# Performance work log

Measured on AMD Instinct MI355X. Metric: run time of the kernel, lower is better.

The kernel has to match this reference:

```python
import math
import jax, jax.numpy as jnp
import numpy as np

B, S, D = 2, 2048, 4096
H, KVH = 32, 8
HD = D // H            # 128
REP = H // KVH         # 4


def setup_inputs() -> dict:
    key = jax.random.key(0)
    ks = jax.random.split(key, 7)
    scale = 1.0 / math.sqrt(D)
    return {
        "x": jax.random.normal(ks[0], (B, S, D), dtype=jnp.float32),
        "freqs_cos": jax.random.uniform(ks[1], (S, HD // 2), dtype=jnp.float32),
        "freqs_sin": jax.random.uniform(ks[2], (S, HD // 2), dtype=jnp.float32),
        "Wq": jax.random.normal(ks[3], (D, H * HD), dtype=jnp.float32) * scale,
        "Wk": jax.random.normal(ks[4], (D, KVH * HD), dtype=jnp.float32) * scale,
        "Wv": jax.random.normal(ks[5], (D, KVH * HD), dtype=jnp.float32) * scale,
        "Wo": jax.random.normal(ks[6], (H * HD, D), dtype=jnp.float32) * scale,
    }


def _rope(t, cos, sin):
    # t: [B,S,h,HD]; pairs are interleaved (reshape to (HD//2, 2) in original)
    tr = t[..., 0::2]
    ti = t[..., 1::2]
    cos = cos[None, :, None, :]  # [1,S,1,HD//2]
    sin = sin[None, :, None, :]
    out_r = tr * cos - ti * sin
    out_i = tr * sin + ti * cos
    return jnp.stack([out_r, out_i], axis=-1).reshape(t.shape)


def reference(x, freqs_cos, freqs_sin, Wq, Wk, Wv, Wo):
    b, s, _ = x.shape
    xq = (x @ Wq).reshape(b, s, H, HD)
    xk = (x @ Wk).reshape(b, s, KVH, HD)
    xv = (x @ Wv).reshape(b, s, KVH, HD)

    xq = _rope(xq, freqs_cos, freqs_sin)
    xk = _rope(xk, freqs_cos, freqs_sin)

    # GQA: repeat each kv head REP times -> [b,s,H,HD]
    xk = jnp.repeat(xk, REP, axis=2)
    xv = jnp.repeat(xv, REP, axis=2)

    q = xq.transpose(0, 2, 1, 3)  # [b,H,s,HD]
    k = xk.transpose(0, 2, 1, 3)
    v = xv.transpose(0, 2, 1, 3)

    scores = jnp.einsum('bhqd,bhkd->bhqk', q, k) / math.sqrt(HD)
    causal = jnp.tril(jnp.ones((s, s), dtype=bool))
    scores = jnp.where(causal[None, None], scores, jnp.float32(-jnp.inf))
    probs = jax.nn.softmax(scores.astype(jnp.float32), axis=-1).astype(x.dtype)

    out = jnp.einsum('bhqk,bhkd->bhqd', probs, v)
    out = out.transpose(0, 2, 1, 3).reshape(b, s, H * HD)
    return out @ Wo
```

## Files before the change

### kernel.cpp

```cpp
#include <hip/hip_runtime.h>

typedef unsigned short u16;
typedef unsigned int u32;
typedef __attribute__((ext_vector_type(8))) short bf16x8;
typedef __attribute__((ext_vector_type(8))) unsigned short u16x8;
typedef __attribute__((ext_vector_type(4))) unsigned short u16x4;
typedef __attribute__((ext_vector_type(4))) float f32x4;
typedef __attribute__((ext_vector_type(4))) unsigned int u32x4;

#define S_LEN 2048
#define NB 2
#define NH 32
#define NKVH 8
#define HD 128
#define DMODEL 4096
#define NEG_BIG (-1.0e30f)

__device__ __forceinline__ float bf2f(u16 x) {
  union { u32 u; float f; } v; v.u = ((u32)x) << 16; return v.f;
}
__device__ __forceinline__ u16 f2bf(float f) {
  union { float f; u32 u; } v; v.f = f;
  u32 r = v.u + 0x7FFFu + ((v.u >> 16) & 1u);
  return (u16)(r >> 16);
}

__global__ __launch_bounds__(256) void transpose_w(const float* __restrict__ W,
                                                   u16* __restrict__ out,
                                                   int N)
{
  __shared__ u16 Ls[64 * 68];
  const int t  = threadIdx.x;
  const int k0 = blockIdx.x * 64;
  const int n0 = blockIdx.y * 64;
#pragma unroll
  for (int i = 0; i < 4; ++i) {
    int kr = (t >> 4) + i * 16;
    int nc = (t & 15) * 4;
    f32x4 v = *(const f32x4*)&W[(size_t)(k0 + kr) * N + n0 + nc];
    u16x4 h = { f2bf(v[0]), f2bf(v[1]), f2bf(v[2]), f2bf(v[3]) };
    *(u16x4*)&Ls[kr * 68 + nc] = h;
  }
  __syncthreads();
#pragma unroll
  for (int i = 0; i < 2; ++i) {
    int nr = (t >> 3) + i * 32;
    int kc = (t & 7) * 8;
    u16x8 h;
#pragma unroll
    for (int j = 0; j < 8; ++j) h[j] = Ls[(kc + j) * 68 + nr];
    *(u16x8*)&out[(size_t)(n0 + nr) * 4096 + k0 + kc] = h;
  }
}

__global__ __launch_bounds__(256) void gemm_qkv(const float* __restrict__ A,
                                                const u16* __restrict__ Bt,
                                                u16* __restrict__ Yq,
                                                u16* __restrict__ Yk,
                                                u16* __restrict__ Yv)
{
  __shared__ u16 As[128 * 40];
  __shared__ u16 Bs[128 * 40];
  const int tid  = threadIdx.x;
  const int wave = tid >> 6;
  const int lane = tid & 63;
  const int lr   = lane & 15;
  const int quad = lane >> 4;
  const int wm   = (wave >> 1) * 64;
  const int wn   = (wave & 1) * 64;
  const int bm   = blockIdx.y * 128;
  const int bn   = blockIdx.x * 128;

  const f32x4 zero = {0.f, 0.f, 0.f, 0.f};
  f32x4 acc[4][4];
#pragma unroll
  for (int i = 0; i < 4; ++i)
#pragma unroll
    for (int j = 0; j < 4; ++j) acc[i][j] = zero;

  for (int kt = 0; kt < 4096; kt += 32) {
    __syncthreads();
#pragma unroll
    for (int i = 0; i < 4; ++i) {
      int e = (tid + i * 256) * 4;
      int row = e >> 5, col = e & 31;
      f32x4 v = *(const f32x4*)&A[(size_t)(bm + row) * 4096 + kt + col];
      u16x4 h = { f2bf(v[0]), f2bf(v[1]), f2bf(v[2]), f2bf(v[3]) };
      *(u16x4*)&As[row * 40 + col] = h;
    }
#pragma unroll
    for (int i = 0; i < 2; ++i) {
      int e = (tid + i * 256) * 8;
      int nr = e >> 5, kc = e & 31;
      *(u32x4*)&Bs[nr * 40 + kc] =
          *(const u32x4*)&Bt[(size_t)(bn + nr) * 4096 + kt + kc];
    }
    __syncthreads();

    bf16x8 af[4], bfr[4];
#pragma unroll
    for (int mt = 0; mt < 4; ++mt)
      af[mt] = *(const bf16x8*)&As[(wm + mt * 16 + lr) * 40 + quad * 8];
#pragma unroll
    for (int nt = 0; nt < 4; ++nt)
      bfr[nt] = *(const bf16x8*)&Bs[(wn + nt * 16 + lr) * 40 + quad * 8];
#pragma unroll
    for (int mt = 0; mt < 4; ++mt)
#pragma unroll
      for (int nt = 0; nt < 4; ++nt)
        acc[mt][nt] = __builtin_amdgcn_mfma_f32_16x16x32_bf16(af[mt], bfr[nt], acc[mt][nt], 0, 0, 0);
  }

  u16* dst; size_t ldc; int nbase;
  if (bn < 4096)      { dst = Yq; ldc = 4096; nbase = bn; }
  else if (bn < 5120) { dst = Yk; ldc = 1024; nbase = bn - 4096; }
  else                { dst = Yv; ldc = 1024; nbase = bn - 5120; }
#pragma unroll
  for (int mt = 0; mt < 4; ++mt)
#pragma unroll
    for (int nt = 0; nt < 4; ++nt)
#pragma unroll
      for (int r = 0; r < 4; ++r) {
        size_t m = (size_t)(bm + wm + mt * 16 + quad * 4 + r);
        size_t n = (size_t)(nbase + wn + nt * 16 + lr);
        dst[m * ldc + n] = f2bf(acc[mt][nt][r]);
      }
}

__global__ __launch_bounds__(256) void gemm_o(const u16* __restrict__ A,
                                              const u16* __restrict__ Bt,
                                              float* __restrict__ C)
{
  __shared__ u16 As[128 * 40];
  __shared__ u16 Bs[128 * 40];
  const int tid  = threadIdx.x;
  const int wave = tid >> 6;
  const int lane = tid & 63;
  const int lr   = lane & 15;
  const int quad = lane >> 4;
  const int wm   = (wave >> 1) * 64;
  const int wn   = (wave & 1) * 64;
  const int bm   = blockIdx.y * 128;
  const int bn   = blockIdx.x * 128;

  const f32x4 zero = {0.f, 0.f, 0.f, 0.f};
  f32x4 acc[4][4];
#pragma unroll
  for (int i = 0; i < 4; ++i)
#pragma unroll
    for (int j = 0; j < 4; ++j) acc[i][j] = zero;

  for (int kt = 0; kt < 4096; kt += 32) {
    __syncthreads();
#pragma unroll
    for (int i = 0; i < 2; ++i) {
      int e = (tid + i * 256) * 8;
      int row = e >> 5, col = e & 31;
      *(u32x4*)&As[row * 40 + col] =
          *(const u32x4*)&A[(size_t)(bm + row) * 4096 + kt + col];
    }
#pragma unroll
    for (int i = 0; i < 2; ++i) {
      int e = (tid + i * 256) * 8;
      int nr = e >> 5, kc = e & 31;
      *(u32x4*)&Bs[nr * 40 + kc] =
          *(const u32x4*)&Bt[(size_t)(bn + nr) * 4096 + kt + kc];
    }
    __syncthreads();

    bf16x8 af[4], bfr[4];
#pragma unroll
    for (int mt = 0; mt < 4; ++mt)
      af[mt] = *(const bf16x8*)&As[(wm + mt * 16 + lr) * 40 + quad * 8];
#pragma unroll
    for (int nt = 0; nt < 4; ++nt)
      bfr[nt] = *(const bf16x8*)&Bs[(wn + nt * 16 + lr) * 40 + quad * 8];
#pragma unroll
    for (int mt = 0; mt < 4; ++mt)
#pragma unroll
      for (int nt = 0; nt < 4; ++nt)
        acc[mt][nt] = __builtin_amdgcn_mfma_f32_16x16x32_bf16(af[mt], bfr[nt], acc[mt][nt], 0, 0, 0);
  }

#pragma unroll
  for (int mt = 0; mt < 4; ++mt)
#pragma unroll
    for (int nt = 0; nt < 4; ++nt)
#pragma unroll
      for (int r = 0; r < 4; ++r) {
        size_t m = (size_t)(bm + wm + mt * 16 + quad * 4 + r);
        size_t n = (size_t)(bn + wn + nt * 16 + lr);
        C[m * 4096 + n] = acc[mt][nt][r];
      }
}

__global__ __launch_bounds__(256) void rope_kernel(u16* __restrict__ Y,
                                                   const float* __restrict__ cp,
                                                   const float* __restrict__ sp,
                                                   int log2nh, int total)
{
  int idx = blockIdx.x * 256 + threadIdx.x;
  if (idx >= total) return;
  int j = idx & 63;
  int s = (idx >> (6 + log2nh)) & (S_LEN - 1);
  u16 t0 = Y[(size_t)idx * 2];
  u16 t1 = Y[(size_t)idx * 2 + 1];
  float tr = bf2f(t0), ti = bf2f(t1);
  float c  = cp[s * 64 + j];
  float sn = sp[s * 64 + j];
  Y[(size_t)idx * 2]     = f2bf(tr * c - ti * sn);
  Y[(size_t)idx * 2 + 1] = f2bf(tr * sn + ti * c);
}

__global__ __launch_bounds__(256) void attn_kernel(const u16* Q,
                                                   const u16* __restrict__ K,
                                                   const u16* __restrict__ V,
                                                   u16* O)
{
  __shared__ u16 Ks[64 * 136];
  __shared__ u16 Vs[128 * 72];
  __shared__ u16 Ps[4 * 16 * 72];

  const int tid  = threadIdx.x;
  const int wave = tid >> 6;
  const int lane = tid & 63;
  const int lr   = lane & 15;
  const int quad = lane >> 4;

  const int b   = blockIdx.z;
  const int h   = blockIdx.y;
  const int q0  = ((int)gridDim.x - 1 - (int)blockIdx.x) * 64;
  const int kvh = h >> 2;

  const int qrow = q0 + wave * 16 + lr;
  const u16* qptr = Q + ((size_t)((b * S_LEN + qrow) * NH + h)) * HD;
  bf16x8 aq[4];
#pragma unroll
  for (int c = 0; c < 4; ++c) aq[c] = *(const bf16x8*)(qptr + c * 32 + quad * 8);

  const f32x4 zero = {0.f, 0.f, 0.f, 0.f};
  f32x4 accO[8];
#pragma unroll
  for (int nt = 0; nt < 8; ++nt) accO[nt] = zero;
  float m_run[4], l_run[4];
#pragma unroll
  for (int r = 0; r < 4; ++r) { m_run[r] = NEG_BIG; l_run[r] = 0.f; }

  const float scale = 0.08838834764831845f;
  const int myq = q0 + wave * 16 + quad * 4;

  for (int kv0 = 0; kv0 <= q0; kv0 += 64) {
    const bool diag = (kv0 == q0);
    __syncthreads();
#pragma unroll
    for (int i = 0; i < 4; ++i) {
      int e = (tid + i * 256) * 8;
      int krow = e >> 7, d0 = e & 127;
      size_t base = ((size_t)((b * S_LEN + kv0 + krow) * NKVH + kvh)) * HD + d0;
      *(u32x4*)&Ks[krow * 136 + d0] = *(const u32x4*)&K[base];
      u16x8 vv = *(const u16x8*)&V[base];
      int kr2 = krow ^ (((d0 >> 3) & 7) << 3);
#pragma unroll
      for (int j = 0; j < 8; ++j) Vs[(d0 + j) * 72 + kr2] = vv[j];
    }
    __syncthreads();

    f32x4 sa[4];
#pragma unroll
    for (int t = 0; t < 4; ++t) {
      f32x4 a = zero;
#pragma unroll
      for (int c = 0; c < 4; ++c) {
        bf16x8 bk = *(const bf16x8*)&Ks[(t * 16 + lr) * 136 + c * 32 + quad * 8];
        a = __builtin_amdgcn_mfma_f32_16x16x32_bf16(aq[c], bk, a, 0, 0, 0);
      }
      sa[t] = a;
    }

    float alpha[4];
#pragma unroll
    for (int r = 0; r < 4; ++r) {
      const int row = myq + r;
      float s[4];
#pragma unroll
      for (int t = 0; t < 4; ++t) {
        float v = sa[t][r] * scale;
        if (diag) v = (kv0 + t * 16 + lr <= row) ? v : NEG_BIG;
        s[t] = v;
      }
      float mx = fmaxf(fmaxf(s[0], s[1]), fmaxf(s[2], s[3]));
#pragma unroll
      for (int off = 8; off >= 1; off >>= 1) mx = fmaxf(mx, __shfl_xor(mx, off));
      float mn = fmaxf(m_run[r], mx);
      alpha[r] = __expf(m_run[r] - mn);
      m_run[r] = mn;
      float p[4], rs = 0.f;
#pragma unroll
      for (int t = 0; t < 4; ++t) { p[t] = __expf(s[t] - mn); rs += p[t]; }
#pragma unroll
      for (int off = 8; off >= 1; off >>= 1) rs += __shfl_xor(rs, off);
      l_run[r] = l_run[r] * alpha[r] + rs;
      const int q  = quad * 4 + r;
      const int sw = (q & 7) << 3;
      const int base = wave * 1152 + q * 72;
#pragma unroll
      for (int t = 0; t < 4; ++t) Ps[base + ((t * 16 + lr) ^ sw)] = f2bf(p[t]);
    }
#pragma unroll
    for (int nt = 0; nt < 8; ++nt)
#pragma unroll
      for (int r = 0; r < 4; ++r) accO[nt][r] *= alpha[r];

#pragma unroll
    for (int kt2 = 0; kt2 < 2; ++kt2) {
      bf16x8 pf = *(const bf16x8*)&Ps[wave * 1152 + lr * 72 +
                                      ((kt2 * 32 + quad * 8) ^ ((lr & 7) << 3))];
#pragma unroll
      for (int nt = 0; nt < 8; ++nt) {
        const int d = nt * 16 + lr;
        bf16x8 vf = *(const bf16x8*)&Vs[d * 72 +
                                        ((kt2 * 32 + quad * 8) ^ (((d >> 3) & 7) << 3))];
        accO[nt] = __builtin_amdgcn_mfma_f32_16x16x32_bf16(pf, vf, accO[nt], 0, 0, 0);
      }
    }
  }

  float rl[4];
#pragma unroll
  for (int r = 0; r < 4; ++r) rl[r] = 1.0f / l_run[r];
#pragma unroll
  for (int nt = 0; nt < 8; ++nt)
#pragma unroll
    for (int r = 0; r < 4; ++r) {
      size_t q = (size_t)(q0 + wave * 16 + quad * 4 + r);
      O[((size_t)b * S_LEN + q) * DMODEL + (size_t)h * HD + nt * 16 + lr] =
          f2bf(accO[nt][r] * rl[r]);
    }
}

extern "C" void kernel_launch(void* const* d_in, const int* in_sizes, int n_in,
                              void* d_out, int out_size, void* d_ws, size_t ws_size,
                              hipStream_t stream)
{
  const float* x  = (const float*)d_in[0];
  const float* cp = (const float*)d_in[1];
  const float* sp = (const float*)d_in[2];
  const float* Wq = (const float*)d_in[3];
  const float* Wk = (const float*)d_in[4];
  const float* Wv = (const float*)d_in[5];
  const float* Wo = (const float*)d_in[6];

  u16* Wt  = (u16*)d_ws;
  u16* Yq  = Wt + (size_t)25165824;
  u16* Yk  = Yq + (size_t)16777216;
  u16* Yv  = Yk + (size_t)4194304;
  u16* att = Yq;
  u16* WoT = Wt;

  transpose_w<<<dim3(64, 64), 256, 0, stream>>>(Wq, Wt,                    4096);
  transpose_w<<<dim3(64, 16), 256, 0, stream>>>(Wk, Wt + (size_t)4096*4096, 1024);
  transpose_w<<<dim3(64, 16), 256, 0, stream>>>(Wv, Wt + (size_t)5120*4096, 1024);
  gemm_qkv<<<dim3(48, 32), 256, 0, stream>>>(x, Wt, Yq, Yk, Yv);
  rope_kernel<<<32768, 256, 0, stream>>>(Yq, cp, sp, 5, 8388608);
  rope_kernel<<<8192, 256, 0, stream>>>(Yk, cp, sp, 3, 2097152);
  attn_kernel<<<dim3(32, 32, 2), 256, 0, stream>>>(Yq, Yk, Yv, att);
  transpose_w<<<dim3(64, 64), 256, 0, stream>>>(Wo, WoT, 4096);
  gemm_o<<<dim3(32, 32), 256, 0, stream>>>(att, WoT, (float*)d_out);
}
```

Before: 1.156 ms.

## Pre-convert x to bf16, use direct global-to-LDS loads in GEMMs, vectorize RoPE

Adds a kernel that converts x to bf16 once, staged in the output buffer, so the QKV GEMM no longer converts fp32 to bf16 in its inner loop. Both GEMMs now fill shared-memory tiles with global_load_lds 16-byte transfers and drop the row padding, which avoids passing the data through registers. RoPE is rewritten to handle 8 elements per thread with vector loads. The unpadded LDS layout may cause more bank conflicts when reading fragments, and the conversion adds an extra pass over x.

```diff
diff --git a/kernel.cpp b/kernel.cpp
--- a/kernel.cpp
+++ b/kernel.cpp
@@ -25,6 +25,23 @@
   return (u16)(r >> 16);
 }
 
+__device__ __forceinline__ void gload16(const void* g, void* l) {
+  __builtin_amdgcn_global_load_lds(
+      (const __attribute__((address_space(1))) void*)g,
+      (__attribute__((address_space(3))) void*)l, 16, 0, 0);
+}
+
+__global__ __launch_bounds__(256) void convert_x(const float* __restrict__ x,
+                                                 u16* __restrict__ xb)
+{
+  int i = blockIdx.x * 256 + threadIdx.x;
+  f32x4 a = *(const f32x4*)&x[(size_t)i * 8];
+  f32x4 b = *(const f32x4*)&x[(size_t)i * 8 + 4];
+  u16x8 h = { f2bf(a[0]), f2bf(a[1]), f2bf(a[2]), f2bf(a[3]),
+              f2bf(b[0]), f2bf(b[1]), f2bf(b[2]), f2bf(b[3]) };
+  *(u16x8*)&xb[(size_t)i * 8] = h;
+}
+
 __global__ __launch_bounds__(256) void transpose_w(const float* __restrict__ W,
                                                    u16* __restrict__ out,
                                                    int N)
@@ -53,14 +70,14 @@
   }
 }
 
-__global__ __launch_bounds__(256) void gemm_qkv(const float* __restrict__ A,
+__global__ __launch_bounds__(256) void gemm_qkv(const u16* __restrict__ A,
                                                 const u16* __restrict__ Bt,
                                                 u16* __restrict__ Yq,
                                                 u16* __restrict__ Yk,
                                                 u16* __restrict__ Yv)
 {
-  __shared__ u16 As[128 * 40];
-  __shared__ u16 Bs[128 * 40];
+  __shared__ u16 As[128 * 32];
+  __shared__ u16 Bs[128 * 32];
   const int tid  = threadIdx.x;
   const int wave = tid >> 6;
   const int lane = tid & 63;
@@ -71,6 +88,11 @@
   const int bm   = blockIdx.y * 128;
   const int bn   = blockIdx.x * 128;
 
+  const int e0  = wave * 1024;
+  const int ra0 = (e0 + lane * 8) >> 5;
+  const int ca0 = (lane & 3) * 8;
+  const int ra1 = ra0 + 16;
+
   const f32x4 zero = {0.f, 0.f, 0.f, 0.f};
   f32x4 acc[4][4];
 #pragma unroll
@@ -80,30 +102,19 @@
 
   for (int kt = 0; kt < 4096; kt += 32) {
     __syncthreads();
-#pragma unroll
-    for (int i = 0; i < 4; ++i) {
-      int e = (tid + i * 256) * 4;
-      int row = e >> 5, col = e & 31;
-      f32x4 v = *(const f32x4*)&A[(size_t)(bm + row) * 4096 + kt + col];
-      u16x4 h = { f2bf(v[0]), f2bf(v[1]), f2bf(v[2]), f2bf(v[3]) };
-      *(u16x4*)&As[row * 40 + col] = h;
-    }
-#pragma unroll
-    for (int i = 0; i < 2; ++i) {
-      int e = (tid + i * 256) * 8;
-      int nr = e >> 5, kc = e & 31;
-      *(u32x4*)&Bs[nr * 40 + kc] =
-          *(const u32x4*)&Bt[(size_t)(bn + nr) * 4096 + kt + kc];
-    }
+    gload16(&A [(size_t)(bm + ra0) * 4096 + kt + ca0], &As[e0]);
+    gload16(&A [(size_t)(bm + ra1) * 4096 + kt + ca0], &As[e0 + 512]);
+    gload16(&Bt[(size_t)(bn + ra0) * 4096 + kt + ca0], &Bs[e0]);
+    gload16(&Bt[(size_t)(bn + ra1) * 4096 + kt + ca0], &Bs[e0 + 512]);
     __syncthreads();
 
     bf16x8 af[4], bfr[4];
 #pragma unroll
     for (int mt = 0; mt < 4; ++mt)
-      af[mt] = *(const bf16x8*)&As[(wm + mt * 16 + lr) * 40 + quad * 8];
+      af[mt] = *(const bf16x8*)&As[(wm + mt * 16 + lr) * 32 + quad * 8];
 #pragma unroll
     for (int nt = 0; nt < 4; ++nt)
-      bfr[nt] = *(const bf16x8*)&Bs[(wn + nt * 16 + lr) * 40 + quad * 8];
+      bfr[nt] = *(const bf16x8*)&Bs[(wn + nt * 16 + lr) * 32 + quad * 8];
 #pragma unroll
     for (int mt = 0; mt < 4; ++mt)
 #pragma unroll
@@ -131,8 +142,8 @@
                                               const u16* __restrict__ Bt,
                                               float* __restrict__ C)
 {
-  __shared__ u16 As[128 * 40];
-  __shared__ u16 Bs[128 * 40];
+  __shared__ u16 As[128 * 32];
+  __shared__ u16 Bs[128 * 32];
   const int tid  = threadIdx.x;
   const int wave = tid >> 6;
   const int lane = tid & 63;
@@ -143,6 +154,11 @@
   const int bm   = blockIdx.y * 128;
   const int bn   = blockIdx.x * 128;
 
+  const int e0  = wave * 1024;
+  const int ra0 = (e0 + lane * 8) >> 5;
+  const int ca0 = (lane & 3) * 8;
+  const int ra1 = ra0 + 16;
+
   const f32x4 zero = {0.f, 0.f, 0.f, 0.f};
   f32x4 acc[4][4];
 #pragma unroll
@@ -152,29 +168,19 @@
 
   for (int kt = 0; kt < 4096; kt += 32) {
     __syncthreads();
-#pragma unroll
-    for (int i = 0; i < 2; ++i) {
-      int e = (tid + i * 256) * 8;
-      int row = e >> 5, col = e & 31;
-      *(u32x4*)&As[row * 40 + col] =
-          *(const u32x4*)&A[(size_t)(bm + row) * 4096 + kt + col];
-    }
-#pragma unroll
-    for (int i = 0; i < 2; ++i) {
-      int e = (tid + i * 256) * 8;
-      int nr = e >> 5, kc = e & 31;
-      *(u32x4*)&Bs[nr * 40 + kc] =
-          *(const u32x4*)&Bt[(size_t)(bn + nr) * 4096 + kt + kc];
-    }
+    gload16(&A [(size_t)(bm + ra0) * 4096 + kt + ca0], &As[e0]);
+    gload16(&A [(size_t)(bm + ra1) * 4096 + kt + ca0], &As[e0 + 512]);
+    gload16(&Bt[(size_t)(bn + ra0) * 4096 + kt + ca0], &Bs[e0]);
+    gload16(&Bt[(size_t)(bn + ra1) * 4096 + kt + ca0], &Bs[e0 + 512]);
     __syncthreads();
 
     bf16x8 af[4], bfr[4];
 #pragma unroll
     for (int mt = 0; mt < 4; ++mt)
-      af[mt] = *(const bf16x8*)&As[(wm + mt * 16 + lr) * 40 + quad * 8];
+      af[mt] = *(const bf16x8*)&As[(wm + mt * 16 + lr) * 32 + quad * 8];
 #pragma unroll
     for (int nt = 0; nt < 4; ++nt)
-      bfr[nt] = *(const bf16x8*)&Bs[(wn + nt * 16 + lr) * 40 + quad * 8];
+      bfr[nt] = *(const bf16x8*)&Bs[(wn + nt * 16 + lr) * 32 + quad * 8];
 #pragma unroll
     for (int mt = 0; mt < 4; ++mt)
 #pragma unroll
@@ -194,22 +200,27 @@
       }
 }
 
-__global__ __launch_bounds__(256) void rope_kernel(u16* __restrict__ Y,
-                                                   const float* __restrict__ cp,
-                                                   const float* __restrict__ sp,
-                                                   int log2nh, int total)
-{
-  int idx = blockIdx.x * 256 + threadIdx.x;
-  if (idx >= total) return;
-  int j = idx & 63;
-  int s = (idx >> (6 + log2nh)) & (S_LEN - 1);
-  u16 t0 = Y[(size_t)idx * 2];
-  u16 t1 = Y[(size_t)idx * 2 + 1];
-  float tr = bf2f(t0), ti = bf2f(t1);
-  float c  = cp[s * 64 + j];
-  float sn = sp[s * 64 + j];
-  Y[(size_t)idx * 2]     = f2bf(tr * c - ti * sn);
-  Y[(size_t)idx * 2 + 1] = f2bf(tr * sn + ti * c);
+__global__ __launch_bounds__(256) void rope_v(u16* __restrict__ Y,
+                                              const float* __restrict__ cp,
+                                              const float* __restrict__ sp,
+                                              int log2nh, int total)
+{
+  int g = blockIdx.x * 256 + threadIdx.x;
+  if (g >= total) return;
+  int j = (g & 15) * 4;
+  int s = (g >> (4 + log2nh)) & (S_LEN - 1);
+  u16x8 t = *(const u16x8*)&Y[(size_t)g * 8];
+  f32x4 c  = *(const f32x4*)&cp[s * 64 + j];
+  f32x4 sn = *(const f32x4*)&sp[s * 64 + j];
+  u16x8 o;
+#pragma unroll
+  for (int p = 0; p < 4; ++p) {
+    float tr = bf2f(t[2 * p]);
+    float ti = bf2f(t[2 * p + 1]);
+    o[2 * p]     = f2bf(tr * c[p] - ti * sn[p]);
+    o[2 * p + 1] = f2bf(tr * sn[p] + ti * c[p]);
+  }
+  *(u16x8*)&Y[(size_t)g * 8] = o;
 }
 
 __global__ __launch_bounds__(256) void attn_kernel(const u16* Q,
@@ -356,13 +367,15 @@
   u16* Yv  = Yk + (size_t)4194304;
   u16* att = Yq;
   u16* WoT = Wt;
+  u16* xb  = (u16*)d_out;
 
   transpose_w<<<dim3(64, 64), 256, 0, stream>>>(Wq, Wt,                    4096);
   transpose_w<<<dim3(64, 16), 256, 0, stream>>>(Wk, Wt + (size_t)4096*4096, 1024);
   transpose_w<<<dim3(64, 16), 256, 0, stream>>>(Wv, Wt + (size_t)5120*4096, 1024);
-  gemm_qkv<<<dim3(48, 32), 256, 0, stream>>>(x, Wt, Yq, Yk, Yv);
-  rope_kernel<<<32768, 256, 0, stream>>>(Yq, cp, sp, 5, 8388608);
-  rope_kernel<<<8192, 256, 0, stream>>>(Yk, cp, sp, 3, 2097152);
+  convert_x<<<8192, 256, 0, stream>>>(x, xb);
+  gemm_qkv<<<dim3(48, 32), 256, 0, stream>>>(xb, Wt, Yq, Yk, Yv);
+  rope_v<<<8192, 256, 0, stream>>>(Yq, cp, sp, 5, 2097152);
+  rope_v<<<2048, 256, 0, stream>>>(Yk, cp, sp, 3, 524288);
   attn_kernel<<<dim3(32, 32, 2), 256, 0, stream>>>(Yq, Yk, Yv, att);
   transpose_w<<<dim3(64, 64), 256, 0, stream>>>(Wo, WoT, 4096);
   gemm_o<<<dim3(32, 32), 256, 0, stream>>>(att, WoT, (float*)d_out);
```

Result: faster. 1.046 ms (-9.5%).
